# Kernel tuning notes

Hardware: AMD Instinct MI355X
Metric: run time of the kernel (lower is better)

The kernel has to match this reference:

```python
import math
import jax, jax.numpy as jnp
import numpy as np

NUM_HEADS = 16
NUM_LANDMARKS = 64


def setup_inputs() -> dict:
    key = jax.random.key(0)
    ks = jax.random.split(key, 14)
    B, S, H, M = 2, 4096, 1024, 512
    p = 0.02
    return {
        "hidden_states": jax.random.normal(ks[0], (B, S, H), jnp.float32),
        "Wq": jax.random.normal(ks[1], (H, H), jnp.float32) * p,
        "bq": jnp.zeros((H,), jnp.float32),
        "Wk": jax.random.normal(ks[2], (H, H), jnp.float32) * p,
        "bk": jnp.zeros((H,), jnp.float32),
        "Wv": jax.random.normal(ks[3], (H, H), jnp.float32) * p,
        "bv": jnp.zeros((H,), jnp.float32),
        "Wo": jax.random.normal(ks[4], (H, H), jnp.float32) * p,
        "bo": jnp.zeros((H,), jnp.float32),
        "mem_keys": jax.random.normal(ks[5], (M, H), jnp.float32) * p,
        "mem_values": jax.random.normal(ks[6], (M, H), jnp.float32) * p,
        "gate_w": jax.random.normal(ks[7], (H, 1), jnp.float32) * p,
        "gate_b": jnp.zeros((1,), jnp.float32),
        "top_k": 32,
    }


def reference(hidden_states, Wq, bq, Wk, bk, Wv, bv, Wo, bo,
              mem_keys, mem_values, gate_w, gate_b, top_k):
    B, S, H = hidden_states.shape
    nh, L = NUM_HEADS, NUM_LANDMARKS
    hd = H // nh

    # ---- landmark selection ('attention' method, no external attn weights) ----
    importance = jnp.linalg.norm(hidden_states, axis=-1)           # [B,S]
    _, lm_idx = jax.lax.top_k(importance, L)                       # [B,L]
    lm_idx = jnp.sort(lm_idx, axis=-1)
    landmark_hidden = jnp.take_along_axis(
        hidden_states, lm_idx[..., None], axis=1)                  # [B,L,H]

    # ---- landmark attention: all tokens attend to L landmarks ----
    q = (hidden_states @ Wq + bq).reshape(B, S, nh, hd)
    k = (landmark_hidden @ Wk + bk).reshape(B, L, nh, hd)
    v = (landmark_hidden @ Wv + bv).reshape(B, L, nh, hd)
    scores = jnp.einsum('bshd,blhd->bhsl', q, k) / math.sqrt(hd)   # [B,nh,S,L]
    attn = jax.nn.softmax(scores, axis=-1)
    ctx = jnp.einsum('bhsl,blhd->bshd', attn, v).reshape(B, S, H)
    landmark_out = ctx @ Wo + bo                                   # [B,S,H]

    # ---- memory bank read (top-k over M memory slots) ----
    mscores = jnp.einsum('bsh,mh->bsm', hidden_states, mem_keys) / math.sqrt(H)
    top_scores, top_idx = jax.lax.top_k(mscores, top_k)            # [B,S,K]
    top_vals = mem_values[top_idx]                                 # [B,S,K,H]
    mattn = jax.nn.softmax(top_scores, axis=-1)
    mem_out = jnp.einsum('bsk,bskh->bsh', mattn, top_vals)         # [B,S,H]
    gate = jax.nn.sigmoid(hidden_states @ gate_w + gate_b)         # [B,S,1]
    mem_out = gate * mem_out

    return landmark_out + mem_out
```

## Files before the change

kernel.cpp:

```cpp
#include <hip/hip_runtime.h>
#include <math.h>

#define HDIM 1024
#define NHEAD 16
#define HD 64
#define LM 64
#define MS 512
#define KSEL 32
#define NB 2
#define NS 4096
#define NTOK (NB*NS)

typedef __attribute__((ext_vector_type(8))) short short8;
typedef __attribute__((ext_vector_type(4))) float f32x4;
typedef __attribute__((ext_vector_type(4))) unsigned short us4;

__device__ __forceinline__ unsigned short f2bf(float f) {
  unsigned int u = __float_as_uint(f);
  unsigned int r = (u + 0x7fffu + ((u >> 16) & 1u)) >> 16;
  return (unsigned short)r;
}
__device__ __forceinline__ float bf2f(unsigned short u) {
  return __uint_as_float(((unsigned int)u) << 16);
}

__device__ __forceinline__ void gload_lds16(const unsigned short* g, unsigned short* l) {
  __builtin_amdgcn_global_load_lds(
      (const __attribute__((address_space(1))) unsigned int*)g,
      (__attribute__((address_space(3))) unsigned int*)l,
      16, 0, 0);
}

#define STAGE64(gbase, k0, LDA, lds)                                          \
  {                                                                           \
    const unsigned short* _s = (gbase) + (k0) + gchk*8;                       \
    gload_lds16(_s,                 (lds) + tid*8);                           \
    gload_lds16(_s + (size_t)32*(LDA), (lds) + 2048 + tid*8);                 \
    gload_lds16(_s + (size_t)64*(LDA), (lds) + 4096 + tid*8);                 \
    gload_lds16(_s + (size_t)96*(LDA), (lds) + 6144 + tid*8);                 \
  }

__global__ __launch_bounds__(256) void imp_gate_kernel(
    const float* __restrict__ hs, const float* __restrict__ gw,
    const float* __restrict__ gb, float* __restrict__ imp,
    float* __restrict__ gate, unsigned short* __restrict__ hsb) {
  const int lane = threadIdx.x & 63, wave = threadIdx.x >> 6;
  const int row = blockIdx.x*4 + wave;
  float ss = 0.f, dg = 0.f;
#pragma unroll
  for (int c = 0; c < 4; ++c) {
    const int d = c*256 + lane*4;
    const float4 hv = *(const float4*)(hs + (size_t)row*HDIM + d);
    const float4 gv = *(const float4*)(gw + d);
    ss += hv.x*hv.x + hv.y*hv.y + hv.z*hv.z + hv.w*hv.w;
    dg += hv.x*gv.x + hv.y*gv.y + hv.z*gv.z + hv.w*gv.w;
    us4 hb;
    hb.x = f2bf(hv.x); hb.y = f2bf(hv.y); hb.z = f2bf(hv.z); hb.w = f2bf(hv.w);
    *(us4*)(hsb + (size_t)row*HDIM + d) = hb;
  }
#pragma unroll
  for (int off = 32; off > 0; off >>= 1) {
    ss += __shfl_xor(ss, off);
    dg += __shfl_xor(dg, off);
  }
  if (lane == 0) {
    imp[row] = ss;
    gate[row] = 1.f/(1.f + expf(-(dg + gb[0])));
  }
}

__global__ __launch_bounds__(256) void lm_count_kernel(
    const float* __restrict__ imp, int* __restrict__ cnt) {
  const int b = blockIdx.z;
  const int jc = blockIdx.y;
  const int i = blockIdx.x*256 + threadIdx.x;
  const float* v = imp + b*NS;
  const float mine = v[i];
  __shared__ float tile[1024];
  const int j0 = jc*1024;
  *(float4*)&tile[threadIdx.x*4] = *(const float4*)&v[j0 + threadIdx.x*4];
  __syncthreads();
  int c = 0;
#pragma unroll 8
  for (int p = 0; p < 1024; p += 4) {
    const float4 t = *(const float4*)&tile[p];
    c += (t.x > mine) || (t.x == mine && (j0+p+0) < i);
    c += (t.y > mine) || (t.y == mine && (j0+p+1) < i);
    c += (t.z > mine) || (t.z == mine && (j0+p+2) < i);
    c += (t.w > mine) || (t.w == mine && (j0+p+3) < i);
  }
  atomicAdd(&cnt[b*NS + i], c);
}

__global__ __launch_bounds__(256) void lm_sel_kernel(
    const int* __restrict__ cnt, int* __restrict__ lm_idx) {
  const int b = blockIdx.y;
  const int i = blockIdx.x*256 + threadIdx.x;
  const int c = cnt[b*NS + i];
  if (c < LM) lm_idx[b*LM + c] = i;
}

__global__ __launch_bounds__(256) void lm_gather_kernel(
    const unsigned short* __restrict__ hsb, const int* __restrict__ lmi,
    unsigned short* __restrict__ g) {
  const int j = blockIdx.x;
  const int b = j >> 6;
  const int idx = lmi[j];
  const us4 v = *(const us4*)(hsb + ((size_t)(b*NS + idx))*HDIM + threadIdx.x*4);
  *(us4*)(g + (size_t)j*HDIM + threadIdx.x*4) = v;
}

__global__ __launch_bounds__(256) void kvproj_gemm_kernel(
    const unsigned short* __restrict__ g, const unsigned short* __restrict__ Wkvt,
    float* __restrict__ part) {
  __shared__ __align__(16) unsigned short As[128*32];
  __shared__ __align__(16) unsigned short Bs[128*32];
  const int tid = threadIdx.x;
  const int lane = tid & 63, wave = tid >> 6;
  const int wr = wave >> 1, wc = wave & 1;
  const int col0 = blockIdx.x << 7;
  const int sp = blockIdx.y;
  const int k00 = sp << 8;

  f32x4 acc[4][4];
#pragma unroll
  for (int m = 0; m < 4; ++m)
#pragma unroll
    for (int n = 0; n < 4; ++n) acc[m][n] = (f32x4)(0.f);

  const int srow = tid >> 2;
  const int sk   = (tid & 3) << 3;
  const unsigned short* gA = g    + (size_t)srow*HDIM + sk;
  const unsigned short* gB = Wkvt + (size_t)(col0 + srow)*HDIM + sk;
  const int fr = lane & 15;
  const int fk = (lane >> 4) << 3;
  const int fg = lane >> 4;

  for (int k0 = k00; k0 < k00 + 256; k0 += 32) {
    gload_lds16(gA + k0,             As + tid*8);
    gload_lds16(gA + 64*HDIM + k0,   As + 2048 + tid*8);
    gload_lds16(gB + k0,             Bs + tid*8);
    gload_lds16(gB + 64*HDIM + k0,   Bs + 2048 + tid*8);
    __syncthreads();
    short8 af[4], bf[4];
#pragma unroll
    for (int m = 0; m < 4; ++m)
      af[m] = *(const short8*)&As[(wr*64 + m*16 + fr)*32 + fk];
#pragma unroll
    for (int n = 0; n < 4; ++n)
      bf[n] = *(const short8*)&Bs[(wc*64 + n*16 + fr)*32 + fk];
#pragma unroll
    for (int m = 0; m < 4; ++m)
#pragma unroll
      for (int n = 0; n < 4; ++n)
        acc[m][n] = __builtin_amdgcn_mfma_f32_16x16x32_bf16(af[m], bf[n], acc[m][n], 0, 0, 0);
    __syncthreads();
  }
#pragma unroll
  for (int m = 0; m < 4; ++m)
#pragma unroll
    for (int n = 0; n < 4; ++n) {
      const int colg = col0 + wc*64 + n*16 + fr;
#pragma unroll
      for (int r = 0; r < 4; ++r) {
        const int row = wr*64 + m*16 + fg*4 + r;
        part[((size_t)(sp*128 + row))*2048 + colg] = acc[m][n][r];
      }
    }
}

__global__ __launch_bounds__(256) void kv_reduce2_kernel(
    const float* __restrict__ part, const float* __restrict__ bk,
    const float* __restrict__ bv, float* __restrict__ kbuf,
    float* __restrict__ vbuf) {
  const int row = blockIdx.y;
  const int col = blockIdx.x*256 + threadIdx.x;
  float s = 0.f;
#pragma unroll
  for (int sp = 0; sp < 4; ++sp)
    s += part[((size_t)(sp*128 + row))*2048 + col];
  if (col < HDIM) kbuf[(size_t)row*HDIM + col] = s + bk[col];
  else            vbuf[(size_t)row*HDIM + col - HDIM] = s + bv[col - HDIM];
}

__global__ __launch_bounds__(256) void prep_kernel(
    const float* __restrict__ Wk, const float* __restrict__ Wv,
    const float* __restrict__ Wq, const float* __restrict__ Wo,
    const float* __restrict__ mk, const float* __restrict__ mv,
    unsigned short* __restrict__ Wkvt, unsigned short* __restrict__ Wcat,
    unsigned short* __restrict__ Wot, unsigned short* __restrict__ mvT) {
  const int z = blockIdx.z;
  __shared__ float tile[32][33];
  const int tx = threadIdx.x & 31, ty = threadIdx.x >> 5;
  if (z < 4) {
    const float* W = (z == 0) ? Wk : (z == 1) ? Wv : (z == 2) ? Wq : Wo;
    unsigned short* Wt = (z == 0) ? Wkvt
                       : (z == 1) ? (Wkvt + (size_t)HDIM*HDIM)
                       : (z == 2) ? Wcat : Wot;
    const int bx = blockIdx.x * 32, by = blockIdx.y * 32;
#pragma unroll
    for (int i = 0; i < 32; i += 8)
      tile[ty + i][tx] = W[(size_t)(by + ty + i)*HDIM + bx + tx];
    __syncthreads();
#pragma unroll
    for (int i = 0; i < 32; i += 8)
      Wt[(size_t)(bx + ty + i)*HDIM + by + tx] = f2bf(tile[tx][ty + i]);
  } else {
    const int blk = blockIdx.y*32 + blockIdx.x;
    if (blk < 512) {
      const int off = (blk << 10) + threadIdx.x*4;
      const float4 v = *(const float4*)&mk[off];
      us4 w;
      w.x = f2bf(v.x); w.y = f2bf(v.y); w.z = f2bf(v.z); w.w = f2bf(v.w);
      *(us4*)&(Wcat + (size_t)HDIM*HDIM)[off] = w;
    } else {
      const int t = blk - 512;
      const int by = (t >> 5) * 32;
      const int bx = (t & 31) * 32;
#pragma unroll
      for (int i = 0; i < 32; i += 8)
        tile[ty + i][tx] = mv[(size_t)(by + ty + i)*HDIM + bx + tx];
      __syncthreads();
#pragma unroll
      for (int i = 0; i < 32; i += 8)
        mvT[(size_t)(bx + ty + i)*MS + by + tx] = f2bf(tile[tx][ty + i]);
    }
  }
}

__global__ __launch_bounds__(256) void gemm_qmsc_kernel(
    const unsigned short* __restrict__ A, const unsigned short* __restrict__ Bt,
    const float* __restrict__ bq, unsigned short* __restrict__ qb,
    float* __restrict__ msc) {
  __shared__ __align__(16) unsigned short As[128*64];
  __shared__ __align__(16) unsigned short Bs[128*64];
  const int tid = threadIdx.x;
  const int lane = tid & 63, wave = tid >> 6;
  const int wr = wave >> 1, wc = wave & 1;
  const int wg = blockIdx.x;
  const int swz = (wg & 7)*96 + (wg >> 3);
  const int bx = swz % 12, by = swz / 12;
  const int row0 = by << 7, col0 = bx << 7;

  f32x4 acc[4][4];
#pragma unroll
  for (int m = 0; m < 4; ++m)
#pragma unroll
    for (int n = 0; n < 4; ++n) acc[m][n] = (f32x4)(0.f);

  const int srow = tid >> 3;
  const int gchk = (tid & 7) ^ (srow & 7);
  const unsigned short* gA = A  + (size_t)(row0 + srow)*HDIM;
  const unsigned short* gB = Bt + (size_t)(col0 + srow)*HDIM;
  const int fr = lane & 15;
  const int fg = lane >> 4;
  const int ca = ((0*4 + fg) ^ (fr & 7)) * 8;
  const int cb = ((1*4 + fg) ^ (fr & 7)) * 8;

  for (int k0 = 0; k0 < HDIM; k0 += 64) {
    STAGE64(gA, k0, HDIM, As);
    STAGE64(gB, k0, HDIM, Bs);
    __syncthreads();
#pragma unroll
    for (int kh = 0; kh < 2; ++kh) {
      const int cc = kh ? cb : ca;
      short8 af[4], bf[4];
#pragma unroll
      for (int m = 0; m < 4; ++m)
        af[m] = *(const short8*)&As[(wr*64 + m*16 + fr)*64 + cc];
#pragma unroll
      for (int n = 0; n < 4; ++n)
        bf[n] = *(const short8*)&Bs[(wc*64 + n*16 + fr)*64 + cc];
#pragma unroll
      for (int m = 0; m < 4; ++m)
#pragma unroll
        for (int n = 0; n < 4; ++n)
          acc[m][n] = __builtin_amdgcn_mfma_f32_16x16x32_bf16(af[m], bf[n], acc[m][n], 0, 0, 0);
    }
    __syncthreads();
  }

#pragma unroll
  for (int m = 0; m < 4; ++m) {
#pragma unroll
    for (int n = 0; n < 4; ++n) {
      const int col = col0 + wc*64 + n*16 + fr;
      if (col < HDIM) {
        const float bb = bq[col];
#pragma unroll
        for (int r = 0; r < 4; ++r) {
          const int row = row0 + wr*64 + m*16 + fg*4 + r;
          qb[(size_t)row*HDIM + col] = f2bf(acc[m][n][r] + bb);
        }
      } else {
        const int c2 = col - HDIM;
#pragma unroll
        for (int r = 0; r < 4; ++r) {
          const int row = row0 + wr*64 + m*16 + fg*4 + r;
          msc[(size_t)row*MS + c2] = acc[m][n][r]*0.03125f;
        }
      }
    }
  }
}

__global__ __launch_bounds__(256) void attn_mfma_kernel(
    const unsigned short* __restrict__ qb, const float* __restrict__ kbuf,
    const float* __restrict__ vbuf, unsigned short* __restrict__ ctxb) {
  const int tb = blockIdx.x, h = blockIdx.y, b = blockIdx.z;
  const int tid = threadIdx.x;
  const int lane = tid & 63, wave = tid >> 6;
  __shared__ __align__(16) unsigned short Qs[128*64];
  __shared__ __align__(16) unsigned short Ks[64*64];
  __shared__ __align__(16) unsigned short Vt[64*64];

  const int tok0 = b*NS + tb*128;
#pragma unroll
  for (int it = 0; it < 4; ++it) {
    const int idx = it*256 + tid;
    gload_lds16(qb + (size_t)(tok0 + (idx >> 3))*HDIM + h*64 + (idx & 7)*8,
                Qs + idx*8);
  }
#pragma unroll
  for (int it = 0; it < 4; ++it) {
    const int i = it*256 + tid;
    const int l = i >> 4, d0 = (i & 15) << 2;
    const size_t base = (size_t)(b*LM + l)*HDIM + h*64 + d0;
    const float4 kv = *(const float4*)(kbuf + base);
    const float4 vv = *(const float4*)(vbuf + base);
    us4 k4; k4.x = f2bf(kv.x); k4.y = f2bf(kv.y); k4.z = f2bf(kv.z); k4.w = f2bf(kv.w);
    *(us4*)&Ks[l*64 + d0] = k4;
    Vt[(d0+0)*64 + l] = f2bf(vv.x);
    Vt[(d0+1)*64 + l] = f2bf(vv.y);
    Vt[(d0+2)*64 + l] = f2bf(vv.z);
    Vt[(d0+3)*64 + l] = f2bf(vv.w);
  }
  __syncthreads();

  const int fr = lane & 15;
  const int fg = lane >> 4;
  const int fk = fg << 3;
  const int wrow = wave*32;

  f32x4 acc[2][4];
#pragma unroll
  for (int m = 0; m < 2; ++m)
#pragma unroll
    for (int n = 0; n < 4; ++n) acc[m][n] = (f32x4)(0.f);
#pragma unroll
  for (int ks = 0; ks < 2; ++ks) {
    short8 af[2], bf[4];
#pragma unroll
    for (int m = 0; m < 2; ++m)
      af[m] = *(const short8*)&Qs[(wrow + m*16 + fr)*64 + ks*32 + fk];
#pragma unroll
    for (int n = 0; n < 4; ++n)
      bf[n] = *(const short8*)&Ks[(n*16 + fr)*64 + ks*32 + fk];
#pragma unroll
    for (int m = 0; m < 2; ++m)
#pragma unroll
      for (int n = 0; n < 4; ++n)
        acc[m][n] = __builtin_amdgcn_mfma_f32_16x16x32_bf16(af[m], bf[n], acc[m][n], 0, 0, 0);
  }

#pragma unroll
  for (int m = 0; m < 2; ++m) {
#pragma unroll
    for (int r = 0; r < 4; ++r) {
      float p0 = acc[m][0][r]*0.125f, p1 = acc[m][1][r]*0.125f;
      float p2 = acc[m][2][r]*0.125f, p3 = acc[m][3][r]*0.125f;
      float mx = fmaxf(fmaxf(p0, p1), fmaxf(p2, p3));
#pragma unroll
      for (int off = 1; off < 16; off <<= 1) mx = fmaxf(mx, __shfl_xor(mx, off));
      p0 = expf(p0 - mx); p1 = expf(p1 - mx); p2 = expf(p2 - mx); p3 = expf(p3 - mx);
      float sm = p0 + p1 + p2 + p3;
#pragma unroll
      for (int off = 1; off < 16; off <<= 1) sm += __shfl_xor(sm, off);
      const float inv = 1.f/sm;
      const int prow = (wrow + m*16 + fg*4 + r)*64;
      Qs[prow + 0*16 + fr] = f2bf(p0*inv);
      Qs[prow + 1*16 + fr] = f2bf(p1*inv);
      Qs[prow + 2*16 + fr] = f2bf(p2*inv);
      Qs[prow + 3*16 + fr] = f2bf(p3*inv);
    }
  }

  f32x4 occ[2][4];
#pragma unroll
  for (int m = 0; m < 2; ++m)
#pragma unroll
    for (int n = 0; n < 4; ++n) occ[m][n] = (f32x4)(0.f);
#pragma unroll
  for (int ks = 0; ks < 2; ++ks) {
    short8 af[2], bf[4];
#pragma unroll
    for (int m = 0; m < 2; ++m)
      af[m] = *(const short8*)&Qs[(wrow + m*16 + fr)*64 + ks*32 + fk];
#pragma unroll
    for (int n = 0; n < 4; ++n)
      bf[n] = *(const short8*)&Vt[(n*16 + fr)*64 + ks*32 + fk];
#pragma unroll
    for (int m = 0; m < 2; ++m)
#pragma unroll
      for (int n = 0; n < 4; ++n)
        occ[m][n] = __builtin_amdgcn_mfma_f32_16x16x32_bf16(af[m], bf[n], occ[m][n], 0, 0, 0);
  }
#pragma unroll
  for (int m = 0; m < 2; ++m)
#pragma unroll
    for (int n = 0; n < 4; ++n)
#pragma unroll
      for (int r = 0; r < 4; ++r)
        ctxb[(size_t)(tok0 + wrow + m*16 + fg*4 + r)*HDIM + h*64 + n*16 + fr] =
            f2bf(occ[m][n][r]);
}

__global__ __launch_bounds__(256) void sel_kernel(
    const float* __restrict__ msc, const float* __restrict__ gate,
    unsigned short* __restrict__ Wm) {
  const int tid = threadIdx.x;
  const int lane = tid & 63, wave = tid >> 6;
  const int token = blockIdx.x*4 + wave;

  __shared__ __align__(16) int s_hist[4][256];
  __shared__ unsigned long long s_list[4][256];
  __shared__ int s_B[4], s_above[4], s_nlist[4];

  *(int4*)&s_hist[wave][lane*4] = make_int4(0, 0, 0, 0);
  if (lane == 0) s_nlist[wave] = 0;

  float v[8];
#pragma unroll
  for (int j = 0; j < 8; ++j) v[j] = msc[(size_t)token*MS + j*64 + lane];

  float mx = v[0], mn = v[0];
#pragma unroll
  for (int j = 1; j < 8; ++j) { mx = fmaxf(mx, v[j]); mn = fminf(mn, v[j]); }
#pragma unroll
  for (int off = 32; off > 0; off >>= 1) {
    mx = fmaxf(mx, __shfl_xor(mx, off));
    mn = fminf(mn, __shfl_xor(mn, off));
  }
  const float range = mx - mn;
  const float scale = (range > 1e-20f) ? 255.f/range : 0.f;

  __builtin_amdgcn_wave_barrier();
  int bins[8];
#pragma unroll
  for (int j = 0; j < 8; ++j) {
    int b = (int)((v[j] - mn)*scale);
    bins[j] = b > 255 ? 255 : b;
    atomicAdd(&s_hist[wave][bins[j]], 1);
  }
  __builtin_amdgcn_wave_barrier();

  const int4 c = *(const int4*)&s_hist[wave][lane*4];
  const int lane_total = c.x + c.y + c.z + c.w;
  int sfx = lane_total;
#pragma unroll
  for (int off = 1; off < 64; off <<= 1) {
    const int src = lane + off;
    int y = __shfl(sfx, src < 64 ? src : lane);
    sfx += (src < 64) ? y : 0;
  }
  const int beyond = sfx - lane_total;
  const int s3 = c.w + beyond;
  const int s2 = c.z + s3;
  const int s1 = c.y + s2;
  const int s0 = c.x + s1;
  int Bl = -1, abv = 0;
  if (s0 >= KSEL && s1 < KSEL) { Bl = lane*4 + 0; abv = s1; }
  if (s1 >= KSEL && s2 < KSEL) { Bl = lane*4 + 1; abv = s2; }
  if (s2 >= KSEL && s3 < KSEL) { Bl = lane*4 + 2; abv = s3; }
  if (s3 >= KSEL && beyond < KSEL) { Bl = lane*4 + 3; abv = beyond; }
  if (Bl >= 0) { s_B[wave] = Bl; s_above[wave] = abv; }
  __builtin_amdgcn_wave_barrier();
  const int B = s_B[wave];
  const int rem = KSEL - s_above[wave];

#pragma unroll
  for (int j = 0; j < 8; ++j) {
    if (bins[j] == B) {
      const unsigned int u = __float_as_uint(v[j]);
      const unsigned int vk = (u & 0x80000000u) ? ~u : (u | 0x80000000u);
      const int p = atomicAdd(&s_nlist[wave], 1);
      if (p < 256)
        s_list[wave][p] = ((unsigned long long)vk << 32) | (unsigned int)~(j*64 + lane);
    }
  }
  __builtin_amdgcn_wave_barrier();

  const int nl = s_nlist[wave] < 256 ? s_nlist[wave] : 256;
  unsigned long long T = ~0ull;
  for (int r = 0; r < rem; ++r) {
    unsigned long long best = 0; int pos = -1;
    for (int i = lane; i < nl; i += 64)
      if (s_list[wave][i] > best) { best = s_list[wave][i]; pos = i; }
#pragma unroll
    for (int off = 32; off > 0; off >>= 1) {
      const unsigned long long ob = __shfl_xor(best, off);
      const int op = __shfl_xor(pos, off);
      if (ob > best) { best = ob; pos = op; }
    }
    if (lane == 0) s_list[wave][pos] = 0;
    T = best;
    __builtin_amdgcn_wave_barrier();
  }

  float e[8];
  float esum = 0.f;
#pragma unroll
  for (int j = 0; j < 8; ++j) {
    bool sel = bins[j] > B;
    if (!sel && bins[j] == B) {
      const unsigned int u = __float_as_uint(v[j]);
      const unsigned int vk = (u & 0x80000000u) ? ~u : (u | 0x80000000u);
      const unsigned long long key =
          ((unsigned long long)vk << 32) | (unsigned int)~(j*64 + lane);
      sel = key >= T;
    }
    e[j] = sel ? expf(v[j] - mx) : 0.f;
    esum += e[j];
  }
#pragma unroll
  for (int off = 32; off > 0; off >>= 1) esum += __shfl_xor(esum, off);
  const float ginv = gate[token]/esum;
#pragma unroll
  for (int j = 0; j < 8; ++j)
    Wm[(size_t)token*MS + j*64 + lane] = f2bf(e[j]*ginv);
}

__global__ __launch_bounds__(256) void gemm_fused_out_kernel(
    const unsigned short* __restrict__ A,
    const unsigned short* __restrict__ Bt,
    const unsigned short* __restrict__ Wm,
    const unsigned short* __restrict__ mvT,
    const float* __restrict__ bias, float* __restrict__ out) {
  __shared__ __align__(16) unsigned short As[128*64];
  __shared__ __align__(16) unsigned short Bs[128*64];
  const int tid = threadIdx.x;
  const int lane = tid & 63, wave = tid >> 6;
  const int wr = wave >> 1, wc = wave & 1;
  const int wg = blockIdx.x;
  const int swz = (wg & 7)*64 + (wg >> 3);
  const int bx = swz & 7, by = swz >> 3;
  const int row0 = by << 7, col0 = bx << 7;

  f32x4 acc[4][4];
#pragma unroll
  for (int m = 0; m < 4; ++m)
#pragma unroll
    for (int n = 0; n < 4; ++n) acc[m][n] = (f32x4)(0.f);

  const int srow = tid >> 3;
  const int gchk = (tid & 7) ^ (srow & 7);
  const int fr = lane & 15;
  const int fg = lane >> 4;
  const int ca = ((0*4 + fg) ^ (fr & 7)) * 8;
  const int cb = ((1*4 + fg) ^ (fr & 7)) * 8;

  {
    const unsigned short* gA = A  + (size_t)(row0 + srow)*HDIM;
    const unsigned short* gB = Bt + (size_t)(col0 + srow)*HDIM;
    for (int k0 = 0; k0 < HDIM; k0 += 64) {
      STAGE64(gA, k0, HDIM, As);
      STAGE64(gB, k0, HDIM, Bs);
      __syncthreads();
#pragma unroll
      for (int kh = 0; kh < 2; ++kh) {
        const int cc = kh ? cb : ca;
        short8 af[4], bf[4];
#pragma unroll
        for (int m = 0; m < 4; ++m)
          af[m] = *(const short8*)&As[(wr*64 + m*16 + fr)*64 + cc];
#pragma unroll
        for (int n = 0; n < 4; ++n)
          bf[n] = *(const short8*)&Bs[(wc*64 + n*16 + fr)*64 + cc];
#pragma unroll
        for (int m = 0; m < 4; ++m)
#pragma unroll
          for (int n = 0; n < 4; ++n)
            acc[m][n] = __builtin_amdgcn_mfma_f32_16x16x32_bf16(af[m], bf[n], acc[m][n], 0, 0, 0);
      }
      __syncthreads();
    }
  }
  {
    const unsigned short* gA = Wm  + (size_t)(row0 + srow)*MS;
    const unsigned short* gB = mvT + (size_t)(col0 + srow)*MS;
    for (int k0 = 0; k0 < MS; k0 += 64) {
      STAGE64(gA, k0, MS, As);
      STAGE64(gB, k0, MS, Bs);
      __syncthreads();
#pragma unroll
      for (int kh = 0; kh < 2; ++kh) {
        const int cc = kh ? cb : ca;
        short8 af[4], bf[4];
#pragma unroll
        for (int m = 0; m < 4; ++m)
          af[m] = *(const short8*)&As[(wr*64 + m*16 + fr)*64 + cc];
#pragma unroll
        for (int n = 0; n < 4; ++n)
          bf[n] = *(const short8*)&Bs[(wc*64 + n*16 + fr)*64 + cc];
#pragma unroll
        for (int m = 0; m < 4; ++m)
#pragma unroll
          for (int n = 0; n < 4; ++n)
            acc[m][n] = __builtin_amdgcn_mfma_f32_16x16x32_bf16(af[m], bf[n], acc[m][n], 0, 0, 0);
      }
      __syncthreads();
    }
  }

#pragma unroll
  for (int m = 0; m < 4; ++m) {
#pragma unroll
    for (int n = 0; n < 4; ++n) {
      const int col = col0 + wc*64 + n*16 + fr;
      const float bb = bias[col];
#pragma unroll
      for (int r = 0; r < 4; ++r) {
        const int row = row0 + wr*64 + m*16 + fg*4 + r;
        out[(size_t)row*HDIM + col] = acc[m][n][r] + bb;
      }
    }
  }
}

extern "C" void kernel_launch(void* const* d_in, const int* in_sizes, int n_in,
                              void* d_out, int out_size, void* d_ws, size_t ws_size,
                              hipStream_t stream) {
  const float* hs = (const float*)d_in[0];
  const float* Wq = (const float*)d_in[1];
  const float* bq = (const float*)d_in[2];
  const float* Wk = (const float*)d_in[3];
  const float* bk = (const float*)d_in[4];
  const float* Wv = (const float*)d_in[5];
  const float* bv = (const float*)d_in[6];
  const float* Wo = (const float*)d_in[7];
  const float* bo = (const float*)d_in[8];
  const float* mk = (const float*)d_in[9];
  const float* mv = (const float*)d_in[10];
  const float* gw = (const float*)d_in[11];
  const float* gb = (const float*)d_in[12];
  float* out = (float*)d_out;

  char* ws = (char*)d_ws;
  unsigned short* hsb  = (unsigned short*)(ws);
  unsigned short* ctxb = hsb;
  unsigned short* qb   = (unsigned short*)(ws + ((size_t)16 << 20));
  unsigned short* Wm   = qb;
  float*          msc  = (float*)(ws + ((size_t)32 << 20));
  unsigned short* Wkvt = (unsigned short*)(ws + ((size_t)48 << 20));
  unsigned short* Wcat = (unsigned short*)(ws + ((size_t)52 << 20));
  unsigned short* Wot  = (unsigned short*)(ws + ((size_t)55 << 20));
  unsigned short* mvT  = (unsigned short*)(ws + ((size_t)57 << 20));
  float*          kbuf = (float*)(ws + ((size_t)58 << 20));
  float*          vbuf = (float*)(ws + ((size_t)58 << 20) + ((size_t)512 << 10));
  unsigned short* g    = (unsigned short*)(ws + ((size_t)59 << 20));
  float*          part = (float*)(ws + ((size_t)59 << 20) + ((size_t)256 << 10));
  float*          imp  = (float*)(ws + ((size_t)64 << 20));
  float*          gate = (float*)(ws + ((size_t)64 << 20) + ((size_t)32 << 10));
  int*            cnt  = (int*)  (ws + ((size_t)64 << 20) + ((size_t)64 << 10));
  int*            lmi  = (int*)  (ws + ((size_t)64 << 20) + ((size_t)96 << 10));

  imp_gate_kernel<<<dim3(NTOK/4), 256, 0, stream>>>(hs, gw, gb, imp, gate, hsb);
  hipMemsetAsync(cnt, 0, NB*NS*sizeof(int), stream);
  lm_count_kernel<<<dim3(NS/256, 4, NB), 256, 0, stream>>>(imp, cnt);
  lm_sel_kernel<<<dim3(NS/256, NB), 256, 0, stream>>>(cnt, lmi);
  prep_kernel<<<dim3(32, 32, 5), 256, 0, stream>>>(
      Wk, Wv, Wq, Wo, mk, mv, Wkvt, Wcat, Wot, mvT);
  lm_gather_kernel<<<dim3(NB*LM), 256, 0, stream>>>(hsb, lmi, g);
  kvproj_gemm_kernel<<<dim3(16, 4), 256, 0, stream>>>(g, Wkvt, part);
  kv_reduce2_kernel<<<dim3(8, 128), 256, 0, stream>>>(part, bk, bv, kbuf, vbuf);
  gemm_qmsc_kernel<<<dim3(768), 256, 0, stream>>>(hsb, Wcat, bq, qb, msc);
  attn_mfma_kernel<<<dim3(NS/128, NHEAD, NB), 256, 0, stream>>>(qb, kbuf, vbuf, ctxb);
  sel_kernel<<<dim3(NTOK/4), 256, 0, stream>>>(msc, gate, Wm);
  gemm_fused_out_kernel<<<dim3(512), 256, 0, stream>>>(ctxb, Wot, Wm, mvT, bo, out);
}
```

Measured before the change: 163.6 us.

## Fuse landmark attention into the Q projection GEMM epilogue

```diff
diff --git a/kernel.cpp b/kernel.cpp
--- a/kernel.cpp
+++ b/kernel.cpp
@@ -171,16 +171,21 @@
 
 __global__ __launch_bounds__(256) void kv_reduce2_kernel(
     const float* __restrict__ part, const float* __restrict__ bk,
-    const float* __restrict__ bv, float* __restrict__ kbuf,
-    float* __restrict__ vbuf) {
+    const float* __restrict__ bv, unsigned short* __restrict__ kbb,
+    unsigned short* __restrict__ vbbT) {
   const int row = blockIdx.y;
   const int col = blockIdx.x*256 + threadIdx.x;
   float s = 0.f;
 #pragma unroll
   for (int sp = 0; sp < 4; ++sp)
     s += part[((size_t)(sp*128 + row))*2048 + col];
-  if (col < HDIM) kbuf[(size_t)row*HDIM + col] = s + bk[col];
-  else            vbuf[(size_t)row*HDIM + col - HDIM] = s + bv[col - HDIM];
+  if (col < HDIM) {
+    kbb[(size_t)row*HDIM + col] = f2bf(s + bk[col]);
+  } else {
+    const int d = col - HDIM;
+    const int b = row >> 6, l = row & 63;
+    vbbT[(size_t)b*65536 + (size_t)d*64 + l] = f2bf(s + bv[d]);
+  }
 }
 
 __global__ __launch_bounds__(256) void prep_kernel(
@@ -228,12 +233,17 @@
   }
 }
 
-__global__ __launch_bounds__(256) void gemm_qmsc_kernel(
-    const unsigned short* __restrict__ A, const unsigned short* __restrict__ Bt,
-    const float* __restrict__ bq, unsigned short* __restrict__ qb,
-    float* __restrict__ msc) {
-  __shared__ __align__(16) unsigned short As[128*64];
-  __shared__ __align__(16) unsigned short Bs[128*64];
+__global__ __launch_bounds__(256, 3) void gemm_qattn_kernel(
+    const unsigned short* __restrict__ A,
+    const unsigned short* __restrict__ Bt,
+    const float* __restrict__ bq,
+    const unsigned short* __restrict__ kbb,
+    const unsigned short* __restrict__ vbbT,
+    unsigned short* __restrict__ ctxb, float* __restrict__ msc) {
+  __shared__ __align__(16) unsigned short As[128*32];
+  __shared__ __align__(16) unsigned short Bs[128*32];
+  __shared__ __align__(16) unsigned short Ks[2*64*64];
+  __shared__ __align__(16) unsigned short Vt[2*64*64];
   const int tid = threadIdx.x;
   const int lane = tid & 63, wave = tid >> 6;
   const int wr = wave >> 1, wc = wave & 1;
@@ -241,6 +251,27 @@
   const int swz = (wg & 7)*96 + (wg >> 3);
   const int bx = swz % 12, by = swz / 12;
   const int row0 = by << 7, col0 = bx << 7;
+  const int fr = lane & 15;
+  const int fk = (lane >> 4) << 3;
+  const int fg = lane >> 4;
+
+  if (bx < 8) {
+    const int b = by >> 5;
+#pragma unroll
+    for (int it = 0; it < 4; ++it) {
+      const int c = it*256 + tid;
+      const int hh = c >> 9, l = (c >> 3) & 63, ch = c & 7;
+      gload_lds16(kbb + (size_t)(b*64 + l)*HDIM + (bx*2 + hh)*64 + ch*8,
+                  Ks + c*8);
+    }
+#pragma unroll
+    for (int it = 0; it < 4; ++it) {
+      const int c = it*256 + tid;
+      const int hh = c >> 9, dr = (c >> 3) & 63, ch = c & 7;
+      gload_lds16(vbbT + (size_t)(by >> 5)*65536 + (size_t)((bx*2 + hh)*64 + dr)*64 + ch*8,
+                  Vt + c*8);
+    }
+  }
 
   f32x4 acc[4][4];
 #pragma unroll
@@ -248,171 +279,141 @@
 #pragma unroll
     for (int n = 0; n < 4; ++n) acc[m][n] = (f32x4)(0.f);
 
-  const int srow = tid >> 3;
-  const int gchk = (tid & 7) ^ (srow & 7);
-  const unsigned short* gA = A  + (size_t)(row0 + srow)*HDIM;
-  const unsigned short* gB = Bt + (size_t)(col0 + srow)*HDIM;
-  const int fr = lane & 15;
-  const int fg = lane >> 4;
-  const int ca = ((0*4 + fg) ^ (fr & 7)) * 8;
-  const int cb = ((1*4 + fg) ^ (fr & 7)) * 8;
-
-  for (int k0 = 0; k0 < HDIM; k0 += 64) {
-    STAGE64(gA, k0, HDIM, As);
-    STAGE64(gB, k0, HDIM, Bs);
+  const int srow = tid >> 2;
+  const int sk   = (tid & 3) << 3;
+  const unsigned short* gA = A  + (size_t)(row0 + srow)*HDIM + sk;
+  const unsigned short* gB = Bt + (size_t)(col0 + srow)*HDIM + sk;
+
+  for (int k0 = 0; k0 < HDIM; k0 += 32) {
+    gload_lds16(gA + k0,             As + tid*8);
+    gload_lds16(gA + 64*HDIM + k0,   As + 2048 + tid*8);
+    gload_lds16(gB + k0,             Bs + tid*8);
+    gload_lds16(gB + 64*HDIM + k0,   Bs + 2048 + tid*8);
     __syncthreads();
-#pragma unroll
-    for (int kh = 0; kh < 2; ++kh) {
-      const int cc = kh ? cb : ca;
-      short8 af[4], bf[4];
-#pragma unroll
-      for (int m = 0; m < 4; ++m)
-        af[m] = *(const short8*)&As[(wr*64 + m*16 + fr)*64 + cc];
+    short8 af[4], bf[4];
+#pragma unroll
+    for (int m = 0; m < 4; ++m)
+      af[m] = *(const short8*)&As[(wr*64 + m*16 + fr)*32 + fk];
+#pragma unroll
+    for (int n = 0; n < 4; ++n)
+      bf[n] = *(const short8*)&Bs[(wc*64 + n*16 + fr)*32 + fk];
+#pragma unroll
+    for (int m = 0; m < 4; ++m)
 #pragma unroll
       for (int n = 0; n < 4; ++n)
-        bf[n] = *(const short8*)&Bs[(wc*64 + n*16 + fr)*64 + cc];
-#pragma unroll
-      for (int m = 0; m < 4; ++m)
-#pragma unroll
-        for (int n = 0; n < 4; ++n)
-          acc[m][n] = __builtin_amdgcn_mfma_f32_16x16x32_bf16(af[m], bf[n], acc[m][n], 0, 0, 0);
-    }
+        acc[m][n] = __builtin_amdgcn_mfma_f32_16x16x32_bf16(af[m], bf[n], acc[m][n], 0, 0, 0);
     __syncthreads();
   }
 
-#pragma unroll
-  for (int m = 0; m < 4; ++m) {
-#pragma unroll
-    for (int n = 0; n < 4; ++n) {
-      const int col = col0 + wc*64 + n*16 + fr;
-      if (col < HDIM) {
-        const float bb = bq[col];
-#pragma unroll
-        for (int r = 0; r < 4; ++r) {
-          const int row = row0 + wr*64 + m*16 + fg*4 + r;
-          qb[(size_t)row*HDIM + col] = f2bf(acc[m][n][r] + bb);
-        }
-      } else {
-        const int c2 = col - HDIM;
+  if (bx >= 8) {
+#pragma unroll
+    for (int m = 0; m < 4; ++m)
+#pragma unroll
+      for (int n = 0; n < 4; ++n) {
+        const int c2 = col0 + wc*64 + n*16 + fr - HDIM;
 #pragma unroll
         for (int r = 0; r < 4; ++r) {
           const int row = row0 + wr*64 + m*16 + fg*4 + r;
           msc[(size_t)row*MS + c2] = acc[m][n][r]*0.03125f;
         }
       }
-    }
-  }
-}
-
-__global__ __launch_bounds__(256) void attn_mfma_kernel(
-    const unsigned short* __restrict__ qb, const float* __restrict__ kbuf,
-    const float* __restrict__ vbuf, unsigned short* __restrict__ ctxb) {
-  const int tb = blockIdx.x, h = blockIdx.y, b = blockIdx.z;
-  const int tid = threadIdx.x;
-  const int lane = tid & 63, wave = tid >> 6;
-  __shared__ __align__(16) unsigned short Qs[128*64];
-  __shared__ __align__(16) unsigned short Ks[64*64];
-  __shared__ __align__(16) unsigned short Vt[64*64];
-
-  const int tok0 = b*NS + tb*128;
-#pragma unroll
-  for (int it = 0; it < 4; ++it) {
-    const int idx = it*256 + tid;
-    gload_lds16(qb + (size_t)(tok0 + (idx >> 3))*HDIM + h*64 + (idx & 7)*8,
-                Qs + idx*8);
-  }
-#pragma unroll
-  for (int it = 0; it < 4; ++it) {
-    const int i = it*256 + tid;
-    const int l = i >> 4, d0 = (i & 15) << 2;
-    const size_t base = (size_t)(b*LM + l)*HDIM + h*64 + d0;
-    const float4 kv = *(const float4*)(kbuf + base);
-    const float4 vv = *(const float4*)(vbuf + base);
-    us4 k4; k4.x = f2bf(kv.x); k4.y = f2bf(kv.y); k4.z = f2bf(kv.z); k4.w = f2bf(kv.w);
-    *(us4*)&Ks[l*64 + d0] = k4;
-    Vt[(d0+0)*64 + l] = f2bf(vv.x);
-    Vt[(d0+1)*64 + l] = f2bf(vv.y);
-    Vt[(d0+2)*64 + l] = f2bf(vv.z);
-    Vt[(d0+3)*64 + l] = f2bf(vv.w);
-  }
-  __syncthreads();
-
-  const int fr = lane & 15;
-  const int fg = lane >> 4;
-  const int fk = fg << 3;
-  const int wrow = wave*32;
-
-  f32x4 acc[2][4];
-#pragma unroll
-  for (int m = 0; m < 2; ++m)
-#pragma unroll
-    for (int n = 0; n < 4; ++n) acc[m][n] = (f32x4)(0.f);
-#pragma unroll
-  for (int ks = 0; ks < 2; ++ks) {
-    short8 af[2], bf[4];
-#pragma unroll
-    for (int m = 0; m < 2; ++m)
-      af[m] = *(const short8*)&Qs[(wrow + m*16 + fr)*64 + ks*32 + fk];
-#pragma unroll
-    for (int n = 0; n < 4; ++n)
-      bf[n] = *(const short8*)&Ks[(n*16 + fr)*64 + ks*32 + fk];
-#pragma unroll
-    for (int m = 0; m < 2; ++m)
+    return;
+  }
+
+  float bqv[4];
+#pragma unroll
+  for (int n = 0; n < 4; ++n) bqv[n] = bq[col0 + wc*64 + n*16 + fr];
+
+  unsigned short* wb = (wave < 2) ? (As + wave*2048) : (Bs + (wave - 2)*2048);
+  const int hb = wc*4096;
+
+#pragma unroll
+  for (int pass = 0; pass < 2; ++pass) {
+#pragma unroll
+    for (int m2 = 0; m2 < 2; ++m2)
 #pragma unroll
       for (int n = 0; n < 4; ++n)
-        acc[m][n] = __builtin_amdgcn_mfma_f32_16x16x32_bf16(af[m], bf[n], acc[m][n], 0, 0, 0);
-  }
-
-#pragma unroll
-  for (int m = 0; m < 2; ++m) {
-#pragma unroll
-    for (int r = 0; r < 4; ++r) {
-      float p0 = acc[m][0][r]*0.125f, p1 = acc[m][1][r]*0.125f;
-      float p2 = acc[m][2][r]*0.125f, p3 = acc[m][3][r]*0.125f;
-      float mx = fmaxf(fmaxf(p0, p1), fmaxf(p2, p3));
-#pragma unroll
-      for (int off = 1; off < 16; off <<= 1) mx = fmaxf(mx, __shfl_xor(mx, off));
-      p0 = expf(p0 - mx); p1 = expf(p1 - mx); p2 = expf(p2 - mx); p3 = expf(p3 - mx);
-      float sm = p0 + p1 + p2 + p3;
-#pragma unroll
-      for (int off = 1; off < 16; off <<= 1) sm += __shfl_xor(sm, off);
-      const float inv = 1.f/sm;
-      const int prow = (wrow + m*16 + fg*4 + r)*64;
-      Qs[prow + 0*16 + fr] = f2bf(p0*inv);
-      Qs[prow + 1*16 + fr] = f2bf(p1*inv);
-      Qs[prow + 2*16 + fr] = f2bf(p2*inv);
-      Qs[prow + 3*16 + fr] = f2bf(p3*inv);
-    }
-  }
-
-  f32x4 occ[2][4];
-#pragma unroll
-  for (int m = 0; m < 2; ++m)
-#pragma unroll
-    for (int n = 0; n < 4; ++n) occ[m][n] = (f32x4)(0.f);
-#pragma unroll
-  for (int ks = 0; ks < 2; ++ks) {
-    short8 af[2], bf[4];
-#pragma unroll
-    for (int m = 0; m < 2; ++m)
-      af[m] = *(const short8*)&Qs[(wrow + m*16 + fr)*64 + ks*32 + fk];
-#pragma unroll
-    for (int n = 0; n < 4; ++n)
-      bf[n] = *(const short8*)&Vt[(n*16 + fr)*64 + ks*32 + fk];
-#pragma unroll
-    for (int m = 0; m < 2; ++m)
+#pragma unroll
+        for (int r = 0; r < 4; ++r)
+          wb[(m2*16 + fg*4 + r)*64 + n*16 + fr] =
+              f2bf(acc[pass*2 + m2][n][r] + bqv[n]);
+    __builtin_amdgcn_wave_barrier();
+
+    f32x4 sc_[2][4];
+#pragma unroll
+    for (int m2 = 0; m2 < 2; ++m2)
+#pragma unroll
+      for (int n = 0; n < 4; ++n) sc_[m2][n] = (f32x4)(0.f);
+#pragma unroll
+    for (int ks = 0; ks < 2; ++ks) {
+      short8 af[2], bf[4];
+#pragma unroll
+      for (int m2 = 0; m2 < 2; ++m2)
+        af[m2] = *(const short8*)&wb[(m2*16 + fr)*64 + ks*32 + fk];
 #pragma unroll
       for (int n = 0; n < 4; ++n)
-        occ[m][n] = __builtin_amdgcn_mfma_f32_16x16x32_bf16(af[m], bf[n], occ[m][n], 0, 0, 0);
-  }
-#pragma unroll
-  for (int m = 0; m < 2; ++m)
-#pragma unroll
-    for (int n = 0; n < 4; ++n)
-#pragma unroll
-      for (int r = 0; r < 4; ++r)
-        ctxb[(size_t)(tok0 + wrow + m*16 + fg*4 + r)*HDIM + h*64 + n*16 + fr] =
-            f2bf(occ[m][n][r]);
+        bf[n] = *(const short8*)&Ks[hb + (n*16 + fr)*64 + ks*32 + fk];
+#pragma unroll
+      for (int m2 = 0; m2 < 2; ++m2)
+#pragma unroll
+        for (int n = 0; n < 4; ++n)
+          sc_[m2][n] = __builtin_amdgcn_mfma_f32_16x16x32_bf16(af[m2], bf[n], sc_[m2][n], 0, 0, 0);
+    }
+
+#pragma unroll
+    for (int m2 = 0; m2 < 2; ++m2) {
+#pragma unroll
+      for (int r = 0; r < 4; ++r) {
+        float p0 = sc_[m2][0][r]*0.125f, p1 = sc_[m2][1][r]*0.125f;
+        float p2 = sc_[m2][2][r]*0.125f, p3 = sc_[m2][3][r]*0.125f;
+        float mx = fmaxf(fmaxf(p0, p1), fmaxf(p2, p3));
+#pragma unroll
+        for (int off = 1; off < 16; off <<= 1) mx = fmaxf(mx, __shfl_xor(mx, off));
+        p0 = expf(p0 - mx); p1 = expf(p1 - mx); p2 = expf(p2 - mx); p3 = expf(p3 - mx);
+        float sm = p0 + p1 + p2 + p3;
+#pragma unroll
+        for (int off = 1; off < 16; off <<= 1) sm += __shfl_xor(sm, off);
+        const float inv = 1.f/sm;
+        const int prow = (m2*16 + fg*4 + r)*64;
+        wb[prow + 0*16 + fr] = f2bf(p0*inv);
+        wb[prow + 1*16 + fr] = f2bf(p1*inv);
+        wb[prow + 2*16 + fr] = f2bf(p2*inv);
+        wb[prow + 3*16 + fr] = f2bf(p3*inv);
+      }
+    }
+    __builtin_amdgcn_wave_barrier();
+
+    f32x4 oc_[2][4];
+#pragma unroll
+    for (int m2 = 0; m2 < 2; ++m2)
+#pragma unroll
+      for (int n = 0; n < 4; ++n) oc_[m2][n] = (f32x4)(0.f);
+#pragma unroll
+    for (int ks = 0; ks < 2; ++ks) {
+      short8 af[2], bf[4];
+#pragma unroll
+      for (int m2 = 0; m2 < 2; ++m2)
+        af[m2] = *(const short8*)&wb[(m2*16 + fr)*64 + ks*32 + fk];
+#pragma unroll
+      for (int n = 0; n < 4; ++n)
+        bf[n] = *(const short8*)&Vt[hb + (n*16 + fr)*64 + ks*32 + fk];
+#pragma unroll
+      for (int m2 = 0; m2 < 2; ++m2)
+#pragma unroll
+        for (int n = 0; n < 4; ++n)
+          oc_[m2][n] = __builtin_amdgcn_mfma_f32_16x16x32_bf16(af[m2], bf[n], oc_[m2][n], 0, 0, 0);
+    }
+#pragma unroll
+    for (int m2 = 0; m2 < 2; ++m2)
+#pragma unroll
+      for (int n = 0; n < 4; ++n)
+#pragma unroll
+        for (int r = 0; r < 4; ++r) {
+          const int tok = row0 + wr*64 + pass*32 + m2*16 + fg*4 + r;
+          ctxb[(size_t)tok*HDIM + col0 + wc*64 + n*16 + fr] = f2bf(oc_[m2][n][r]);
+        }
+    __builtin_amdgcn_wave_barrier();
+  }
 }
 
 __global__ __launch_bounds__(256) void sel_kernel(
@@ -647,22 +648,21 @@
 
   char* ws = (char*)d_ws;
   unsigned short* hsb  = (unsigned short*)(ws);
-  unsigned short* ctxb = hsb;
-  unsigned short* qb   = (unsigned short*)(ws + ((size_t)16 << 20));
-  unsigned short* Wm   = qb;
+  unsigned short* ctxb = (unsigned short*)(ws + ((size_t)16 << 20));
   float*          msc  = (float*)(ws + ((size_t)32 << 20));
-  unsigned short* Wkvt = (unsigned short*)(ws + ((size_t)48 << 20));
-  unsigned short* Wcat = (unsigned short*)(ws + ((size_t)52 << 20));
-  unsigned short* Wot  = (unsigned short*)(ws + ((size_t)55 << 20));
-  unsigned short* mvT  = (unsigned short*)(ws + ((size_t)57 << 20));
-  float*          kbuf = (float*)(ws + ((size_t)58 << 20));
-  float*          vbuf = (float*)(ws + ((size_t)58 << 20) + ((size_t)512 << 10));
-  unsigned short* g    = (unsigned short*)(ws + ((size_t)59 << 20));
-  float*          part = (float*)(ws + ((size_t)59 << 20) + ((size_t)256 << 10));
-  float*          imp  = (float*)(ws + ((size_t)64 << 20));
-  float*          gate = (float*)(ws + ((size_t)64 << 20) + ((size_t)32 << 10));
-  int*            cnt  = (int*)  (ws + ((size_t)64 << 20) + ((size_t)64 << 10));
-  int*            lmi  = (int*)  (ws + ((size_t)64 << 20) + ((size_t)96 << 10));
+  unsigned short* Wm   = (unsigned short*)(ws + ((size_t)48 << 20));
+  unsigned short* Wkvt = (unsigned short*)(ws + ((size_t)56 << 20));
+  unsigned short* Wcat = (unsigned short*)(ws + ((size_t)60 << 20));
+  unsigned short* Wot  = (unsigned short*)(ws + ((size_t)63 << 20));
+  unsigned short* mvT  = (unsigned short*)(ws + ((size_t)65 << 20));
+  unsigned short* kbb  = (unsigned short*)(ws + ((size_t)66 << 20));
+  unsigned short* vbbT = (unsigned short*)(ws + ((size_t)66 << 20) + ((size_t)256 << 10));
+  unsigned short* g    = (unsigned short*)(ws + ((size_t)66 << 20) + ((size_t)512 << 10));
+  float*          part = (float*)(ws + ((size_t)67 << 20));
+  float*          imp  = (float*)(ws + ((size_t)71 << 20));
+  float*          gate = (float*)(ws + ((size_t)71 << 20) + ((size_t)32 << 10));
+  int*            cnt  = (int*)  (ws + ((size_t)71 << 20) + ((size_t)64 << 10));
+  int*            lmi  = (int*)  (ws + ((size_t)71 << 20) + ((size_t)96 << 10));
 
   imp_gate_kernel<<<dim3(NTOK/4), 256, 0, stream>>>(hs, gw, gb, imp, gate, hsb);
   hipMemsetAsync(cnt, 0, NB*NS*sizeof(int), stream);
@@ -672,9 +672,8 @@
       Wk, Wv, Wq, Wo, mk, mv, Wkvt, Wcat, Wot, mvT);
   lm_gather_kernel<<<dim3(NB*LM), 256, 0, stream>>>(hsb, lmi, g);
   kvproj_gemm_kernel<<<dim3(16, 4), 256, 0, stream>>>(g, Wkvt, part);
-  kv_reduce2_kernel<<<dim3(8, 128), 256, 0, stream>>>(part, bk, bv, kbuf, vbuf);
-  gemm_qmsc_kernel<<<dim3(768), 256, 0, stream>>>(hsb, Wcat, bq, qb, msc);
-  attn_mfma_kernel<<<dim3(NS/128, NHEAD, NB), 256, 0, stream>>>(qb, kbuf, vbuf, ctxb);
+  kv_reduce2_kernel<<<dim3(8, 128), 256, 0, stream>>>(part, bk, bv, kbb, vbbT);
+  gemm_qattn_kernel<<<dim3(768), 256, 0, stream>>>(hsb, Wcat, bq, kbb, vbbT, ctxb, msc);
   sel_kernel<<<dim3(NTOK/4), 256, 0, stream>>>(msc, gate, Wm);
   gemm_fused_out_kernel<<<dim3(512), 256, 0, stream>>>(ctxb, Wot, Wm, mvT, bo, out);
 }
```

Result: faster. 147.1 us (-10.1%).
